# Performance work log

Measured on AMD Instinct MI355X. Metric: run time of the kernel, lower is better.

Reference implementation:

```python
import jax, jax.numpy as jnp
import numpy as np

N = 50000      # nodes
E = 800000     # edges (before self-loops)
DIN = 146      # input feature dim
D = 128        # hidden/out dim
G = 64         # graphs in batch
L = 4          # number of GCNConv layers (len(hidden_dims[1:]) + 1)
NC = 10        # classes
EPS = 1e-5     # BatchNorm eps


def setup_inputs() -> dict:
    key = jax.random.key(0)
    ks = jax.random.split(key, 12)
    x = jax.random.normal(ks[0], (N, DIN), jnp.float32)
    edge_index = jax.random.randint(ks[1], (2, E), 0, N, dtype=jnp.int64)
    batch = jnp.sort(jax.random.randint(ks[2], (N,), 0, G, dtype=jnp.int64))

    def lin(k, shape, fan_in):
        return (jax.random.normal(k, shape, jnp.float32) / np.sqrt(fan_in)).astype(jnp.float32)

    W_emb = lin(ks[3], (DIN, D), DIN)
    b_emb = jnp.zeros((D,), jnp.float32)
    W_gcn = lin(ks[4], (L, D, D), D)
    b_gcn = jnp.zeros((L, D), jnp.float32)
    bn_gamma = jnp.ones((L, D), jnp.float32)
    bn_beta = jnp.zeros((L, D), jnp.float32)
    W_r1 = lin(ks[5], (D, D // 2), D)
    b_r1 = jnp.zeros((D // 2,), jnp.float32)
    W_r2 = lin(ks[6], (D // 2, D // 4), D // 2)
    b_r2 = jnp.zeros((D // 4,), jnp.float32)
    W_r3 = lin(ks[7], (D // 4, NC), D // 4)
    b_r3 = jnp.zeros((NC,), jnp.float32)
    return {"x": x, "edge_index": edge_index, "batch": batch,
            "W_emb": W_emb, "b_emb": b_emb, "W_gcn": W_gcn, "b_gcn": b_gcn,
            "bn_gamma": bn_gamma, "bn_beta": bn_beta,
            "W_r1": W_r1, "b_r1": b_r1, "W_r2": W_r2, "b_r2": b_r2,
            "W_r3": W_r3, "b_r3": b_r3}


def reference(x, edge_index, batch, W_emb, b_emb, W_gcn, b_gcn,
              bn_gamma, bn_beta, W_r1, b_r1, W_r2, b_r2, W_r3, b_r3):
    # gcn_norm with self-loops (fill_value=1, improved=False)
    loop = jnp.arange(N, dtype=edge_index.dtype)
    src = jnp.concatenate([edge_index[0], loop])
    dst = jnp.concatenate([edge_index[1], loop])
    deg = jax.ops.segment_sum(jnp.ones(src.shape, x.dtype), dst, num_segments=N)
    dinv = jax.lax.rsqrt(jnp.maximum(deg, jnp.asarray(1e-12, x.dtype)))  # deg >= 1 (self loops)
    norm = (dinv[src] * dinv[dst])[:, None]  # [E+N, 1]

    h = x @ W_emb + b_emb  # embedding_h
    for l in range(L):
        h_in = h
        m = h @ W_gcn[l]                                            # [N, D]
        h = jax.ops.segment_sum(m[src] * norm, dst, num_segments=N) + b_gcn[l]
        # BatchNorm1d (training-mode batch stats, biased var)
        mu = h.mean(axis=0)
        var = h.var(axis=0)
        h = (h - mu) * jax.lax.rsqrt(var + EPS) * bn_gamma[l] + bn_beta[l]
        h = jax.nn.relu(h)
        h = h_in + h  # residual (dims always match here)

    # global_mean_pool over batch ids
    sums = jax.ops.segment_sum(h, batch, num_segments=G)
    cnts = jax.ops.segment_sum(jnp.ones((N, 1), h.dtype), batch, num_segments=G)
    hg = sums / jnp.maximum(cnts, 1.0)

    # MLPReadout: two hidden layers halving dims, then classifier
    z = jax.nn.relu(hg @ W_r1 + b_r1)
    z = jax.nn.relu(z @ W_r2 + b_r2)
    return z @ W_r3 + b_r3  # [G, NC]
```

## Files before the change

### kernel.cpp

```cpp
#include <hip/hip_runtime.h>
#include <hip/hip_bf16.h>

#define NN 50000
#define EE 800000
#define DIN 146
#define DD 128
#define GG 64
#define LL 4
#define NC 10
#define BN_EPS 1e-5f

#define KP_EMB 160
#define AST_L  136
#define NCOPY 64
#define NPW 2

#define NBKT 196
#define BHP  200
#define NBE  782

#define A_EDGE   NBE
#define A_INIT   (A_EDGE + 256)
#define A_REPACK (A_INIT + 3907)
#define A_BATCH  (A_REPACK + 196)
#define A_PARAMS (A_BATCH + 384)
#define A_WT     (A_PARAMS + 400)

#define B_GEMM 391
#define C_TOT  (B_GEMM + NBE)

typedef __attribute__((ext_vector_type(8))) short bf16x8;
typedef __attribute__((ext_vector_type(4))) float f32x4;

__device__ __forceinline__ float bf2f(__hip_bfloat16 v) { return __bfloat162float(v); }
__device__ __forceinline__ float loadf(const void* p, long i, int f32) {
    return f32 ? ((const float*)p)[i] : bf2f(((const __hip_bfloat16*)p)[i]);
}
__device__ __forceinline__ unsigned short f2bf_bits(float f) {
    __hip_bfloat16 h = __float2bfloat16(f);
    return *(unsigned short*)&h;
}
__device__ __forceinline__ float bfu2f(unsigned short u) {
    return __uint_as_float((unsigned)u << 16);
}
__device__ __forceinline__ float lo16(unsigned v) { return __uint_as_float(v << 16); }
__device__ __forceinline__ float hi16(unsigned v) { return __uint_as_float(v & 0xffff0000u); }
__device__ __forceinline__ float sload_f(const float* __restrict__ p, int j) {
    return __uint_as_float(__builtin_amdgcn_readfirstlane(__float_as_uint(p[j])));
}
__device__ __forceinline__ ushort4 pack4(f32x4 v) {
    ushort4 u;
    u.x = f2bf_bits(v[0]); u.y = f2bf_bits(v[1]);
    u.z = f2bf_bits(v[2]); u.w = f2bf_bits(v[3]);
    return u;
}

__device__ __forceinline__ int blk_excl_scan(int v, int t, int* wsum, int* total_sh) {
    __syncthreads();
    int lane = t & 63, w = t >> 6;
    int x = v;
    #pragma unroll
    for (int s = 1; s < 64; s <<= 1) {
        int y = __shfl_up(x, s, 64);
        if (lane >= s) x += y;
    }
    if (lane == 63) wsum[w] = x;
    __syncthreads();
    if (t == 0) {
// ... 244 lines not shown
    for (int t8 = 0; t8 < 8; ++t8) {
        #pragma unroll
        for (int c = 0; c < 5; ++c) {
            bf16x8 b = *(const bf16x8*)(Wt + (long)(t8 * 16 + m) * KP_EMB + c * 32 + quad * 8);
            acc[0][t8] = __builtin_amdgcn_mfma_f32_16x16x32_bf16(b, a[0][c], acc[0][t8], 0, 0, 0);
            acc[1][t8] = __builtin_amdgcn_mfma_f32_16x16x32_bf16(b, a[1][c], acc[1][t8], 0, 0, 0);
        }
    }
    #pragma unroll
    for (int rt = 0; rt < 2; ++rt) {
        int row = rbase + rt * 16 + m;
        int rloc = rl + rt * 16 + m;
        #pragma unroll
        for (int t8 = 0; t8 < 8; ++t8) {
            ushort4 u = pack4(acc[rt][t8]);
            *(ushort4*)(&sh.As[rloc * AST_L + t8 * 16 + quad * 4]) = u;
            if (row < n)
                *(ushort4*)(hb + (long)row * DD + t8 * 16 + quad * 4) = u;
        }
    }
    __syncthreads();
    bf16x8 a2[2][4];
    #pragma unroll
    for (int rt = 0; rt < 2; ++rt)
        #pragma unroll
        for (int c = 0; c < 4; ++c)
            a2[rt][c] = *(const bf16x8*)(&sh.As[(rl + rt * 16 + m) * AST_L + c * 32 + quad * 8]);
    f32x4 acc2[2][8];
    #pragma unroll
    for (int t8 = 0; t8 < 8; ++t8) {
        f32x4 z = {0.f, 0.f, 0.f, 0.f};
        acc2[0][t8] = z; acc2[1][t8] = z;
    }
    #pragma unroll
    for (int t8 = 0; t8 < 8; ++t8) {
        #pragma unroll
        for (int c = 0; c < 4; ++c) {
            bf16x8 b = *(const bf16x8*)(Wt0 + (long)(t8 * 16 + m) * DD + c * 32 + quad * 8);
            acc2[0][t8] = __builtin_amdgcn_mfma_f32_16x16x32_bf16(b, a2[0][c], acc2[0][t8], 0, 0, 0);
            acc2[1][t8] = __builtin_amdgcn_mfma_f32_16x16x32_bf16(b, a2[1][c], acc2[1][t8], 0, 0, 0);
        }
    }
    #pragma unroll
    for (int rt = 0; rt < 2; ++rt) {
        int row = rbase + rt * 16 + m;
        if (row < n) {
            #pragma unroll
            for (int t8 = 0; t8 < 8; ++t8)
                *(ushort4*)(Mb + (long)row * DD + t8 * 16 + quad * 4) = pack4(acc2[rt][t8]);
        }
    }
}

__global__ __launch_bounds__(256) void csr_kernel(
    const unsigned* __restrict__ bucketA, const int* __restrict__ base,
    int* __restrict__ off, float* __restrict__ dinv, int* __restrict__ src_s)
{
    __shared__ int dg[256], cur[256], wsum[4], total_sh;
    int b = blockIdx.x, t = threadIdx.x;
    int eb0 = base[b], eb1 = base[b + 1];
    dg[t] = 0;
    __syncthreads();
    for (int e = eb0 + t; e < eb1; e += 256)
        atomicAdd(&dg[bucketA[e] & 255u], 1);
    __syncthreads();
    int v = dg[t];
    int excl = blk_excl_scan(v, t, wsum, &total_sh);
    int node = b * 256 + t;
    if (node < NN) {
        off[node] = eb0 + excl;
        dinv[node] = rsqrtf((float)(v + 1));
    }
    cur[t] = excl;
    __syncthreads();
    for (int e = eb0 + t; e < eb1; e += 256) {
        unsigned pv = bucketA[e];
        int r = atomicAdd(&cur[pv & 255u], 1);
        src_s[eb0 + r] = (int)(pv >> 8);
    }
}

__global__ __launch_bounds__(256) void gemm_fused_kernel(
    const unsigned short* __restrict__ aggb, unsigned short* __restrict__ hb,
    const float* __restrict__ statmulti, const float* __restrict__ gamma,
    const float* __restrict__ beta,
    const unsigned short* __restrict__ Wt, unsigned short* __restrict__ Mb, int n)
{
    __shared__ unsigned short As[128 * AST_L];
    __shared__ float bnsh[256];
    int t = threadIdx.x;
    int r0 = blockIdx.x * 128;
    {
        float s = 0.0f;
        #pragma unroll 8
        for (int k = 0; k < NCOPY; ++k) s += statmulti[k * 256 + t];
        bnsh[t] = s;
    }
    __syncthreads();
    {
        int c4 = (t & 31) * 4, rsub = t >> 5;
        float inv_n = 1.0f / (float)n;
        float4 sm = *(const float4*)&bnsh[c4];
        float4 sq = *(const float4*)&bnsh[128 + c4];
        float4 ga = *(const float4*)&gamma[c4];
        float4 be = *(const float4*)&beta[c4];
        float4 mu, rs;
        mu.x = sm.x * inv_n; mu.y = sm.y * inv_n; mu.z = sm.z * inv_n; mu.w = sm.w * inv_n;
        rs.x = rsqrtf(sq.x * inv_n - mu.x * mu.x + BN_EPS) * ga.x;
        rs.y = rsqrtf(sq.y * inv_n - mu.y * mu.y + BN_EPS) * ga.y;
        rs.z = rsqrtf(sq.z * inv_n - mu.z * mu.z + BN_EPS) * ga.z;
        rs.w = rsqrtf(sq.w * inv_n - mu.w * mu.w + BN_EPS) * ga.w;
        #pragma unroll 4
        for (int i = 0; i < 16; ++i) {
            int row = i * 8 + rsub;
            int r = r0 + row;
            unsigned short o0 = 0, o1 = 0, o2 = 0, o3 = 0;
            if (r < n) {
                long g = (long)r * DD + c4;
                ushort4 au = *(const ushort4*)&aggb[g];
                ushort4 hu = *(const ushort4*)&hb[g];
                float h0 = bfu2f(hu.x) + fmaxf((bfu2f(au.x) - mu.x) * rs.x + be.x, 0.0f);
                float h1 = bfu2f(hu.y) + fmaxf((bfu2f(au.y) - mu.y) * rs.y + be.y, 0.0f);
                float h2 = bfu2f(hu.z) + fmaxf((bfu2f(au.z) - mu.z) * rs.z + be.z, 0.0f);
                float h3 = bfu2f(hu.w) + fmaxf((bfu2f(au.w) - mu.w) * rs.w + be.w, 0.0f);
                o0 = f2bf_bits(h0); o1 = f2bf_bits(h1);
                o2 = f2bf_bits(h2); o3 = f2bf_bits(h3);
                ushort4 ho; ho.x = o0; ho.y = o1; ho.z = o2; ho.w = o3;
                *(ushort4*)&hb[g] = ho;
            }
            unsigned short* dst = &As[row * AST_L + c4];
            dst[0] = o0; dst[1] = o1; dst[2] = o2; dst[3] = o3;
        }
    }
    __syncthreads();
    int lane = t & 63, w = t >> 6;
    int m = lane & 15, quad = lane >> 4;
    int rl = w * 32;
    int rbase = r0 + rl;
    bf16x8 a[2][4];
    #pragma unroll
    for (int rt = 0; rt < 2; ++rt)
        #pragma unroll
        for (int c = 0; c < 4; ++c)
            a[rt][c] = *(const bf16x8*)(As + (rl + rt * 16 + m) * AST_L + c * 32 + quad * 8);
    f32x4 acc[2][8];
    #pragma unroll
    for (int t8 = 0; t8 < 8; ++t8) {
        f32x4 z = {0.f, 0.f, 0.f, 0.f};
        acc[0][t8] = z; acc[1][t8] = z;
    }
    #pragma unroll
    for (int t8 = 0; t8 < 8; ++t8) {
        #pragma unroll
        for (int c = 0; c < 4; ++c) {
            bf16x8 b = *(const bf16x8*)(Wt + (long)(t8 * 16 + m) * DD + c * 32 + quad * 8);
            acc[0][t8] = __builtin_amdgcn_mfma_f32_16x16x32_bf16(b, a[0][c], acc[0][t8], 0, 0, 0);
            acc[1][t8] = __builtin_amdgcn_mfma_f32_16x16x32_bf16(b, a[1][c], acc[1][t8], 0, 0, 0);
        }
    }
    #pragma unroll
    for (int rt = 0; rt < 2; ++rt) {
        int row = rbase + rt * 16 + m;
        if (row < n) {
            #pragma unroll
            for (int t8 = 0; t8 < 8; ++t8)
                *(ushort4*)(Mb + (long)row * DD + t8 * 16 + quad * 4) = pack4(acc[rt][t8]);
        }
    }
}

__global__ __launch_bounds__(256) void agg_kernel(
    const unsigned* __restrict__ mb32, const int* __restrict__ off,
    const int* __restrict__ src_s,
    const float* __restrict__ dinv, const float* __restrict__ bias,
    unsigned* __restrict__ aggb32, float* __restrict__ statacc)
{
    __shared__ float2 ssum[4][64], ssq[4][64];
    int t = threadIdx.x;
    int wv = t >> 6, lane = t & 63;
    float2 bi = ((const float2*)bias)[lane];
    float2 sAcc = {0.0f, 0.0f}, qAcc = {0.0f, 0.0f};
    int i0 = (blockIdx.x * 4 + wv) * NPW;
    #pragma unroll 1
    for (int ni = 0; ni < NPW; ++ni) {
        int i = i0 + ni;
        if (i >= NN) break;
        int e  = __builtin_amdgcn_readfirstlane(off[i]);
        int e1 = __builtin_amdgcn_readfirstlane(off[i + 1]);
        float di = sload_f(dinv, i);
        unsigned vs = mb32[(long)i * 64 + lane];
        float a0 = di * lo16(vs), a1 = di * hi16(vs);
        for (; e + 8 <= e1; e += 8) {
            int j0 = __builtin_amdgcn_readfirstlane(src_s[e + 0]);
            int j1 = __builtin_amdgcn_readfirstlane(src_s[e + 1]);
            int j2 = __builtin_amdgcn_readfirstlane(src_s[e + 2]);
            int j3 = __builtin_amdgcn_readfirstlane(src_s[e + 3]);
            int j4 = __builtin_amdgcn_readfirstlane(src_s[e + 4]);
            int j5 = __builtin_amdgcn_readfirstlane(src_s[e + 5]);
            int j6 = __builtin_amdgcn_readfirstlane(src_s[e + 6]);
            int j7 = __builtin_amdgcn_readfirstlane(src_s[e + 7]);
            float d0 = sload_f(dinv, j0), d1 = sload_f(dinv, j1);
            float d2 = sload_f(dinv, j2), d3 = sload_f(dinv, j3);
            float d4 = sload_f(dinv, j4), d5 = sload_f(dinv, j5);
            float d6 = sload_f(dinv, j6), d7 = sload_f(dinv, j7);
            unsigned v0 = mb32[(long)j0 * 64 + lane];
            unsigned v1 = mb32[(long)j1 * 64 + lane];
            unsigned v2 = mb32[(long)j2 * 64 + lane];
            unsigned v3 = mb32[(long)j3 * 64 + lane];
            unsigned v4 = mb32[(long)j4 * 64 + lane];
            unsigned v5 = mb32[(long)j5 * 64 + lane];
            unsigned v6 = mb32[(long)j6 * 64 + lane];
            unsigned v7 = mb32[(long)j7 * 64 + lane];
            a0 = fmaf(d0, lo16(v0), a0); a1 = fmaf(d0, hi16(v0), a1);
            a0 = fmaf(d1, lo16(v1), a0); a1 = fmaf(d1, hi16(v1), a1);
            a0 = fmaf(d2, lo16(v2), a0); a1 = fmaf(d2, hi16(v2), a1);
            a0 = fmaf(d3, lo16(v3), a0); a1 = fmaf(d3, hi16(v3), a1);
            a0 = fmaf(d4, lo16(v4), a0); a1 = fmaf(d4, hi16(v4), a1);
            a0 = fmaf(d5, lo16(v5), a0); a1 = fmaf(d5, hi16(v5), a1);
            a0 = fmaf(d6, lo16(v6), a0); a1 = fmaf(d6, hi16(v6), a1);
            a0 = fmaf(d7, lo16(v7), a0); a1 = fmaf(d7, hi16(v7), a1);
        }
        for (; e + 4 <= e1; e += 4) {
            int j0 = __builtin_amdgcn_readfirstlane(src_s[e + 0]);
            int j1 = __builtin_amdgcn_readfirstlane(src_s[e + 1]);
            int j2 = __builtin_amdgcn_readfirstlane(src_s[e + 2]);
            int j3 = __builtin_amdgcn_readfirstlane(src_s[e + 3]);
            float d0 = sload_f(dinv, j0), d1 = sload_f(dinv, j1);
            float d2 = sload_f(dinv, j2), d3 = sload_f(dinv, j3);
            unsigned v0 = mb32[(long)j0 * 64 + lane];
            unsigned v1 = mb32[(long)j1 * 64 + lane];
            unsigned v2 = mb32[(long)j2 * 64 + lane];
            unsigned v3 = mb32[(long)j3 * 64 + lane];
            a0 = fmaf(d0, lo16(v0), a0); a1 = fmaf(d0, hi16(v0), a1);
            a0 = fmaf(d1, lo16(v1), a0); a1 = fmaf(d1, hi16(v1), a1);
            a0 = fmaf(d2, lo16(v2), a0); a1 = fmaf(d2, hi16(v2), a1);
            a0 = fmaf(d3, lo16(v3), a0); a1 = fmaf(d3, hi16(v3), a1);
        }
        for (; e < e1; ++e) {
            int j = __builtin_amdgcn_readfirstlane(src_s[e]);
            float dj = sload_f(dinv, j);
            unsigned v = mb32[(long)j * 64 + lane];
            a0 = fmaf(dj, lo16(v), a0); a1 = fmaf(dj, hi16(v), a1);
        }
        float o0 = fmaf(di, a0, bi.x);
        float o1 = fmaf(di, a1, bi.y);
        aggb32[(long)i * 64 + lane] = ((unsigned)f2bf_bits(o1) << 16) | f2bf_bits(o0);
        sAcc.x += o0; sAcc.y += o1;
        qAcc.x += o0 * o0; qAcc.y += o1 * o1;
    }
    ssum[wv][lane] = sAcc; ssq[wv][lane] = qAcc;
    __syncthreads();
    if (wv == 0) {
        float2 s0 = ssum[0][lane], s1 = ssum[1][lane], s2 = ssum[2][lane], s3 = ssum[3][lane];
        float2 q0 = ssq[0][lane], q1 = ssq[1][lane], q2 = ssq[2][lane], q3 = ssq[3][lane];
        float sx = s0.x + s1.x + s2.x + s3.x;
        float sy = s0.y + s1.y + s2.y + s3.y;
        float qx = q0.x + q1.x + q2.x + q3.x;
        float qy = q0.y + q1.y + q2.y + q3.y;
        float* copy = statacc + (blockIdx.x & (NCOPY - 1)) * 256;
        atomicAdd(&copy[2 * lane], sx);
        atomicAdd(&copy[2 * lane + 1], sy);
        atomicAdd(&copy[128 + 2 * lane], qx);
        atomicAdd(&copy[128 + 2 * lane + 1], qy);
    }
}

__global__ void pool1_kernel(const unsigned short* __restrict__ hb,
                             const unsigned short* __restrict__ aggb,
                             const float* __restrict__ statmulti,
                             const float* __restrict__ gamma, const float* __restrict__ beta,
                             const int* __restrict__ b32, float* __restrict__ hgsum, int n) {
    __shared__ float bnsh[256];
    int t = threadIdx.x;
    {
        float s = 0.0f;
        #pragma unroll 8
        for (int k = 0; k < NCOPY; ++k) s += statmulti[k * 256 + t];
        bnsh[t] = s;
    }
    __syncthreads();
    int c4 = (t & 31) * 4, rsub = t >> 5;
    float inv_n = 1.0f / (float)n;
    float4 sm = *(const float4*)&bnsh[c4];
    float4 sq = *(const float4*)&bnsh[128 + c4];
    float4 ga = *(const float4*)&gamma[c4];
    float4 be = *(const float4*)&beta[c4];
    float4 mu, rs;
    mu.x = sm.x * inv_n; mu.y = sm.y * inv_n; mu.z = sm.z * inv_n; mu.w = sm.w * inv_n;
    rs.x = rsqrtf(sq.x * inv_n - mu.x * mu.x + BN_EPS) * ga.x;
    rs.y = rsqrtf(sq.y * inv_n - mu.y * mu.y + BN_EPS) * ga.y;
    rs.z = rsqrtf(sq.z * inv_n - mu.z * mu.z + BN_EPS) * ga.z;
    rs.w = rsqrtf(sq.w * inv_n - mu.w * mu.w + BN_EPS) * ga.w;
    int rows_pb = (n + gridDim.x - 1) / gridDim.x;
    int r0 = blockIdx.x * rows_pb;
    int r1 = min(n, r0 + rows_pb);
    float4 acc = {0, 0, 0, 0};
    int gcur = -1;
    for (int r = r0 + rsub; r < r1; r += 8) {
        int g = b32[r];
        if (g != gcur) {
            if (gcur >= 0) {
                atomicAdd(&hgsum[gcur * DD + c4 + 0], acc.x);
                atomicAdd(&hgsum[gcur * DD + c4 + 1], acc.y);
                atomicAdd(&hgsum[gcur * DD + c4 + 2], acc.z);
                atomicAdd(&hgsum[gcur * DD + c4 + 3], acc.w);
            }
            acc.x = acc.y = acc.z = acc.w = 0.0f;
            gcur = ((unsigned)g < (unsigned)GG) ? g : -1;
        }
        if (gcur >= 0) {
            long ix = (long)r * DD + c4;
            ushort4 au = *(const ushort4*)&aggb[ix];
            ushort4 hu = *(const ushort4*)&hb[ix];
            acc.x += bfu2f(hu.x) + fmaxf((bfu2f(au.x) - mu.x) * rs.x + be.x, 0.0f);
            acc.y += bfu2f(hu.y) + fmaxf((bfu2f(au.y) - mu.y) * rs.y + be.y, 0.0f);
            acc.z += bfu2f(hu.z) + fmaxf((bfu2f(au.z) - mu.z) * rs.z + be.z, 0.0f);
            acc.w += bfu2f(hu.w) + fmaxf((bfu2f(au.w) - mu.w) * rs.w + be.w, 0.0f);
        }
    }
    if (gcur >= 0) {
        atomicAdd(&hgsum[gcur * DD + c4 + 0], acc.x);
        atomicAdd(&hgsum[gcur * DD + c4 + 1], acc.y);
        atomicAdd(&hgsum[gcur * DD + c4 + 2], acc.z);
        atomicAdd(&hgsum[gcur * DD + c4 + 3], acc.w);
    }
}

__device__ int lower_bound_i(const int* __restrict__ a, int n, int v) {
    int lo = 0, hi = n;
    while (lo < hi) {
        int mid = (lo + hi) >> 1;
        if (a[mid] < v) lo = mid + 1; else hi = mid;
    }
    return lo;
}

__global__ void readout_kernel(const float* __restrict__ hgsum, const int* __restrict__ b32,
                               const float* __restrict__ W1, const float* __restrict__ b1,
                               const float* __restrict__ W2, const float* __restrict__ b2,
                               const float* __restrict__ W3, const float* __restrict__ b3,
                               const int* __restrict__ flags, void* __restrict__ out, int n) {
    int f32 = flags[2];
    int g = blockIdx.x;
    int t = threadIdx.x;
    __shared__ float hgs[DD];
    __shared__ float z1[DD / 2];
    __shared__ float z2[DD / 4];
    int lo = lower_bound_i(b32, n, g);
    int hi = lower_bound_i(b32, n, g + 1);
    float invc = 1.0f / fmaxf((float)(hi - lo), 1.0f);
    hgs[t] = hgsum[g * DD + t] * invc;
    __syncthreads();
    if (t < DD / 2) {
        float acc = b1[t];
        #pragma unroll 8
        for (int k = 0; k < DD; ++k) acc = fmaf(hgs[k], W1[k * (DD / 2) + t], acc);
        z1[t] = fmaxf(acc, 0.0f);
    }
    __syncthreads();
    if (t < DD / 4) {
        float acc = b2[t];
        #pragma unroll 8
        for (int k = 0; k < DD / 2; ++k) acc = fmaf(z1[k], W2[k * (DD / 4) + t], acc);
        z2[t] = fmaxf(acc, 0.0f);
    }
    __syncthreads();
    if (t < NC) {
        float acc = b3[t];
        #pragma unroll 8
        for (int k = 0; k < DD / 4; ++k) acc = fmaf(z2[k], W3[k * NC + t], acc);
        if (f32) ((float*)out)[g * NC + t] = acc;
        else     ((__hip_bfloat16*)out)[g * NC + t] = __float2bfloat16(acc);
    }
}

extern "C" void kernel_launch(void* const* d_in, const int* in_sizes, int n_in,
                              void* d_out, int out_size, void* d_ws, size_t ws_size,
                              hipStream_t stream) {
    const void* x      = d_in[0];
    const void* ei     = d_in[1];
    const void* batch  = d_in[2];
    const void* W_emb  = d_in[3];
    const void* b_emb  = d_in[4];
    const void* W_gcn  = d_in[5];
    const void* b_gcn  = d_in[6];
    const void* bn_g   = d_in[7];
    const void* bn_b   = d_in[8];
    const void* W_r1   = d_in[9];
    const void* b_r1   = d_in[10];
    const void* W_r2   = d_in[11];
    const void* b_r2   = d_in[12];
    const void* W_r3   = d_in[13];
    const void* b_r3   = d_in[14];

    char* p = (char*)d_ws;
    auto alloc = [&](size_t bytes) -> void* {
        void* r = (void*)p;
        p += (bytes + 255) & ~(size_t)255;
        return r;
    };
    int*   flags  = (int*)alloc(64 * 4);
    int*   dcnt   = (int*)alloc(64 * 4);
    float* statmulti = (float*)alloc((size_t)LL * NCOPY * 256 * 4);
    float* hgsum  = (float*)alloc((size_t)GG * DD * 4);
    int*   off    = (int*)alloc((size_t)(NN + 1) * 4);
    float* dinv   = (float*)alloc((size_t)NN * 4);
    int*   b32    = (int*)alloc((size_t)NN * 4);
    int*   src_s  = (int*)alloc((size_t)EE * 4);
    unsigned* pk  = (unsigned*)alloc((size_t)EE * 4);
    unsigned char* bkt = (unsigned char*)alloc((size_t)EE);
    int*   bh     = (int*)alloc((size_t)NBE * BHP * 4);
    int*   tot    = (int*)alloc(256 * 4);
    int*   base   = (int*)alloc(256 * 4);
    unsigned* bucketA = (unsigned*)alloc((size_t)EE * 4);
    unsigned short* hb = (unsigned short*)alloc((size_t)NN * DD * 2);
    unsigned short* mb = (unsigned short*)alloc((size_t)NN * DD * 2);
    unsigned short* aggb = (unsigned short*)alloc((size_t)NN * DD * 2);
    unsigned short* xb = (unsigned short*)alloc((size_t)NN * KP_EMB * 2);
    unsigned short* wt_emb = (unsigned short*)alloc((size_t)DD * KP_EMB * 2);
    unsigned short* wt_gcn = (unsigned short*)alloc((size_t)LL * DD * DD * 2);
    float* b_emb32 = (float*)alloc(DD * 4);
    float* b_gcn32 = (float*)alloc((size_t)LL * DD * 4);
    float* bng32   = (float*)alloc((size_t)LL * DD * 4);
    float* bnb32   = (float*)alloc((size_t)LL * DD * 4);
    float* wr1     = (float*)alloc((size_t)DD * (DD / 2) * 4);
    float* br1     = (float*)alloc((DD / 2) * 4);
    float* wr2     = (float*)alloc((size_t)(DD / 2) * (DD / 4) * 4);
    float* br2     = (float*)alloc((DD / 4) * 4);
    float* wr3     = (float*)alloc((size_t)(DD / 4) * NC * 4);
    float* br3     = (float*)alloc(NC * 4);

    detect_kernel<<<1, 64, 0, stream>>>(ei, batch, W_emb, flags);

    Params12 P;
    P.p[0]  = { b_emb, b_emb32, DD, DD };
    P.p[1]  = { b_gcn, b_gcn32, LL * DD, LL * DD };
    P.p[2]  = { bn_g,  bng32,   LL * DD, LL * DD };
    P.p[3]  = { bn_b,  bnb32,   LL * DD, LL * DD };
    P.p[4]  = { W_r1,  wr1,     DD * (DD / 2), DD * (DD / 2) };
    P.p[5]  = { b_r1,  br1,     DD / 2, DD / 2 };
    P.p[6]  = { W_r2,  wr2,     (DD / 2) * (DD / 4), (DD / 2) * (DD / 4) };
    P.p[7]  = { b_r2,  br2,     DD / 4, DD / 4 };
    P.p[8]  = { W_r3,  wr3,     (DD / 4) * NC, (DD / 4) * NC };
    P.p[9]  = { b_r3,  br3,     NC, NC };
    P.p[10] = { b_r3,  br3,     0, 0 };
    P.p[11] = { b_r3,  br3,     0, 0 };

    WtDescs5 W;
    W.p[0] = { W_emb, 0,            wt_emb,                DIN, KP_EMB };
    W.p[1] = { W_gcn, 0L * DD * DD, wt_gcn + 0L * DD * DD, DD,  DD };
    W.p[2] = { W_gcn, 1L * DD * DD, wt_gcn + 1L * DD * DD, DD,  DD };
    W.p[3] = { W_gcn, 2L * DD * DD, wt_gcn + 2L * DD * DD, DD,  DD };
    W.p[4] = { W_gcn, 3L * DD * DD, wt_gcn + 3L * DD * DD, DD,  DD };

    mega_conv_kernel<<<A_WT, 256, 0, stream>>>(x, ei, batch, flags, xb, statmulti,
                                               hgsum, b32, pk, bkt, bh, dcnt, P, W);

    bscan_kernel<<<NBKT, 256, 0, stream>>>(bh, tot, base, off + NN, dcnt);

    bucket_emb_kernel<<<C_TOT, 256, 0, stream>>>(pk, bkt, bh, base, bucketA,
                                                 xb, wt_emb, wt_gcn, b_emb32, hb, mb, NN);

    csr_kernel<<<NBKT, 256, 0, stream>>>(bucketA, base, off, dinv, src_s);

    int ngemm = (NN + 127) / 128;
    int nagg = (NN + 4 * NPW - 1) / (4 * NPW);
    for (int l = 0; l < LL; ++l) {
        if (l > 0) {
            gemm_fused_kernel<<<ngemm, 256, 0, stream>>>(
                aggb, hb, statmulti + (size_t)(l - 1) * NCOPY * 256,
                bng32 + (l - 1) * DD, bnb32 + (l - 1) * DD,
                wt_gcn + (size_t)l * DD * DD, mb, NN);
        }
        agg_kernel<<<nagg, 256, 0, stream>>>((const unsigned*)mb, off, src_s, dinv,
                                             b_gcn32 + l * DD, (unsigned*)aggb,
                                             statmulti + (size_t)l * NCOPY * 256);
    }

    pool1_kernel<<<512, 256, 0, stream>>>(hb, aggb, statmulti + (size_t)(LL - 1) * NCOPY * 256,
                                          bng32 + (LL - 1) * DD, bnb32 + (LL - 1) * DD,
                                          b32, hgsum, NN);
    readout_kernel<<<GG, DD, 0, stream>>>(hgsum, b32, wr1, br1, wr2, br2, wr3, br3,
                                          flags, d_out, NN);
}
```

Measured before the change: 405.8 us.

## Fuse CSR build, GCN layers, pooling and readout into one cooperative persistent kernel

```diff
diff --git a/kernel.cpp b/kernel.cpp
--- a/kernel.cpp
+++ b/kernel.cpp
@@ -1,5 +1,8 @@
 #include <hip/hip_runtime.h>
 #include <hip/hip_bf16.h>
+#include <hip/hip_cooperative_groups.h>
+
+namespace cg = cooperative_groups;
 
 #define NN 50000
 #define EE 800000
@@ -13,7 +16,7 @@
 #define KP_EMB 160
 #define AST_L  136
 #define NCOPY 64
-#define NPW 2
+#define NT_GEMM 391
 
 #define NBKT 196
 #define BHP  200
@@ -364,56 +367,263 @@
     }
 }
 
-__global__ __launch_bounds__(256) void csr_kernel(
-    const unsigned* __restrict__ bucketA, const int* __restrict__ base,
-    int* __restrict__ off, float* __restrict__ dinv, int* __restrict__ src_s)
-{
-    __shared__ int dg[256], cur[256], wsum[4], total_sh;
-    int b = blockIdx.x, t = threadIdx.x;
-    int eb0 = base[b], eb1 = base[b + 1];
-    dg[t] = 0;
-    __syncthreads();
-    for (int e = eb0 + t; e < eb1; e += 256)
-        atomicAdd(&dg[bucketA[e] & 255u], 1);
-    __syncthreads();
-    int v = dg[t];
-    int excl = blk_excl_scan(v, t, wsum, &total_sh);
-    int node = b * 256 + t;
-    if (node < NN) {
-        off[node] = eb0 + excl;
-        dinv[node] = rsqrtf((float)(v + 1));
-    }
-    cur[t] = excl;
-    __syncthreads();
-    for (int e = eb0 + t; e < eb1; e += 256) {
-        unsigned pv = bucketA[e];
-        int r = atomicAdd(&cur[pv & 255u], 1);
-        src_s[eb0 + r] = (int)(pv >> 8);
-    }
-}
-
-__global__ __launch_bounds__(256) void gemm_fused_kernel(
-    const unsigned short* __restrict__ aggb, unsigned short* __restrict__ hb,
-    const float* __restrict__ statmulti, const float* __restrict__ gamma,
-    const float* __restrict__ beta,
-    const unsigned short* __restrict__ Wt, unsigned short* __restrict__ Mb, int n)
-{
-    __shared__ unsigned short As[128 * AST_L];
-    __shared__ float bnsh[256];
+__device__ __forceinline__ int lower_bound_i(const int* __restrict__ a, int n, int v) {
+    int lo = 0, hi = n;
+    while (lo < hi) {
+        int mid = (lo + hi) >> 1;
+        if (a[mid] < v) lo = mid + 1; else hi = mid;
+    }
+    return lo;
+}
+
+struct LayersArgs {
+    const unsigned* bucketA; const int* base;
+    int* off; float* dinv; int* src_s;
+    unsigned short* aggb; unsigned short* hb;
+    float* statmulti;
+    const float* bng; const float* bnb;
+    const unsigned short* wt_gcn;
+    unsigned short* mb;
+    const float* bgcn;
+    const int* b32; float* hgsum;
+    const float* W1; const float* b1; const float* W2; const float* b2;
+    const float* W3; const float* b3;
+    const int* flags; void* out; int n;
+};
+
+__global__ __launch_bounds__(256, 3) void layers_kernel(LayersArgs A) {
+    cg::grid_group grid = cg::this_grid();
+    __shared__ union {
+        struct { unsigned short As[128 * AST_L]; float bnsh[256]; } g;
+        struct { float2 ssum[4][64]; float2 ssq[4][64]; } a;
+        struct { int dg[256]; int cur[256]; int wsum[4]; int total; } c;
+        struct { float hgs[DD]; float z1[DD / 2]; float z2[DD / 4]; } r;
+    } sh;
     int t = threadIdx.x;
-    int r0 = blockIdx.x * 128;
+    int n = A.n;
+    int lane = t & 63, wv = t >> 6;
+    int m = lane & 15, quad = lane >> 4;
+    int rl = wv * 32;
+
+    for (int b = blockIdx.x; b < NBKT; b += gridDim.x) {
+        int eb0 = A.base[b], eb1 = A.base[b + 1];
+        sh.c.dg[t] = 0;
+        __syncthreads();
+        for (int e = eb0 + t; e < eb1; e += 256)
+            atomicAdd(&sh.c.dg[A.bucketA[e] & 255u], 1);
+        __syncthreads();
+        int v = sh.c.dg[t];
+        int excl = blk_excl_scan(v, t, sh.c.wsum, &sh.c.total);
+        int node = b * 256 + t;
+        if (node < NN) {
+            A.off[node] = eb0 + excl;
+            A.dinv[node] = rsqrtf((float)(v + 1));
+        }
+        sh.c.cur[t] = excl;
+        __syncthreads();
+        for (int e = eb0 + t; e < eb1; e += 256) {
+            unsigned pv = A.bucketA[e];
+            int r = atomicAdd(&sh.c.cur[pv & 255u], 1);
+            A.src_s[eb0 + r] = (int)(pv >> 8);
+        }
+        __syncthreads();
+    }
+    grid.sync();
+
+    const unsigned* mb32 = (const unsigned*)A.mb;
+    unsigned* aggb32 = (unsigned*)A.aggb;
+
+    for (int l = 0; l < LL; ++l) {
+        if (l > 0) {
+            const float* statm = A.statmulti + (size_t)(l - 1) * NCOPY * 256;
+            const float* gamma = A.bng + (size_t)(l - 1) * DD;
+            const float* beta  = A.bnb + (size_t)(l - 1) * DD;
+            const unsigned short* Wt = A.wt_gcn + (size_t)l * DD * DD;
+            {
+                float s = 0.0f;
+                #pragma unroll 8
+                for (int k = 0; k < NCOPY; ++k) s += statm[k * 256 + t];
+                sh.g.bnsh[t] = s;
+            }
+            __syncthreads();
+            int c4 = (t & 31) * 4, rsub = t >> 5;
+            float inv_n = 1.0f / (float)n;
+            float4 sm = *(const float4*)&sh.g.bnsh[c4];
+            float4 sq = *(const float4*)&sh.g.bnsh[128 + c4];
+            float4 ga = *(const float4*)&gamma[c4];
+            float4 be = *(const float4*)&beta[c4];
+            float4 mu, rs;
+            mu.x = sm.x * inv_n; mu.y = sm.y * inv_n; mu.z = sm.z * inv_n; mu.w = sm.w * inv_n;
+            rs.x = rsqrtf(sq.x * inv_n - mu.x * mu.x + BN_EPS) * ga.x;
+            rs.y = rsqrtf(sq.y * inv_n - mu.y * mu.y + BN_EPS) * ga.y;
+            rs.z = rsqrtf(sq.z * inv_n - mu.z * mu.z + BN_EPS) * ga.z;
+            rs.w = rsqrtf(sq.w * inv_n - mu.w * mu.w + BN_EPS) * ga.w;
+            for (int tile = blockIdx.x; tile < NT_GEMM; tile += gridDim.x) {
+                int r0 = tile * 128;
+                __syncthreads();
+                #pragma unroll 4
+                for (int i = 0; i < 16; ++i) {
+                    int row = i * 8 + rsub;
+                    int r = r0 + row;
+                    unsigned short o0 = 0, o1 = 0, o2 = 0, o3 = 0;
+                    if (r < n) {
+                        long g = (long)r * DD + c4;
+                        ushort4 au = *(const ushort4*)&A.aggb[g];
+                        ushort4 hu = *(const ushort4*)&A.hb[g];
+                        float h0 = bfu2f(hu.x) + fmaxf((bfu2f(au.x) - mu.x) * rs.x + be.x, 0.0f);
+                        float h1 = bfu2f(hu.y) + fmaxf((bfu2f(au.y) - mu.y) * rs.y + be.y, 0.0f);
+                        float h2 = bfu2f(hu.z) + fmaxf((bfu2f(au.z) - mu.z) * rs.z + be.z, 0.0f);
+                        float h3 = bfu2f(hu.w) + fmaxf((bfu2f(au.w) - mu.w) * rs.w + be.w, 0.0f);
+                        o0 = f2bf_bits(h0); o1 = f2bf_bits(h1);
+                        o2 = f2bf_bits(h2); o3 = f2bf_bits(h3);
+                        ushort4 ho; ho.x = o0; ho.y = o1; ho.z = o2; ho.w = o3;
+                        *(ushort4*)&A.hb[g] = ho;
+                    }
+                    unsigned short* dst = &sh.g.As[row * AST_L + c4];
+                    dst[0] = o0; dst[1] = o1; dst[2] = o2; dst[3] = o3;
+                }
+                __syncthreads();
+                int rbase = r0 + rl;
+                bf16x8 a[2][4];
+                #pragma unroll
+                for (int rt = 0; rt < 2; ++rt)
+                    #pragma unroll
+                    for (int c = 0; c < 4; ++c)
+                        a[rt][c] = *(const bf16x8*)(&sh.g.As[(rl + rt * 16 + m) * AST_L + c * 32 + quad * 8]);
+                f32x4 acc[2][8];
+                #pragma unroll
+                for (int t8 = 0; t8 < 8; ++t8) {
+                    f32x4 z = {0.f, 0.f, 0.f, 0.f};
+                    acc[0][t8] = z; acc[1][t8] = z;
+                }
+                #pragma unroll
+                for (int t8 = 0; t8 < 8; ++t8) {
+                    #pragma unroll
+                    for (int c = 0; c < 4; ++c) {
+                        bf16x8 b = *(const bf16x8*)(Wt + (long)(t8 * 16 + m) * DD + c * 32 + quad * 8);
+                        acc[0][t8] = __builtin_amdgcn_mfma_f32_16x16x32_bf16(b, a[0][c], acc[0][t8], 0, 0, 0);
+                        acc[1][t8] = __builtin_amdgcn_mfma_f32_16x16x32_bf16(b, a[1][c], acc[1][t8], 0, 0, 0);
+                    }
+                }
+                #pragma unroll
+                for (int rt = 0; rt < 2; ++rt) {
+                    int row = rbase + rt * 16 + m;
+                    if (row < n) {
+                        #pragma unroll
+                        for (int t8 = 0; t8 < 8; ++t8)
+                            *(ushort4*)(A.mb + (long)row * DD + t8 * 16 + quad * 4) = pack4(acc[rt][t8]);
+                    }
+                }
+            }
+            grid.sync();
+        }
+        {
+            const float* bias = A.bgcn + (size_t)l * DD;
+            float* statacc = A.statmulti + (size_t)l * NCOPY * 256;
+            float2 bi = ((const float2*)bias)[lane];
+            float2 sAcc = {0.0f, 0.0f}, qAcc = {0.0f, 0.0f};
+            int wstep = gridDim.x * 4;
+            for (int i = blockIdx.x * 4 + wv; i < n; i += wstep) {
+                int e  = __builtin_amdgcn_readfirstlane(A.off[i]);
+                int e1 = __builtin_amdgcn_readfirstlane(A.off[i + 1]);
+                float di = sload_f(A.dinv, i);
+                unsigned vs = mb32[(long)i * 64 + lane];
+                float a0 = di * lo16(vs), a1 = di * hi16(vs);
+                for (; e + 8 <= e1; e += 8) {
+                    int j0 = __builtin_amdgcn_readfirstlane(A.src_s[e + 0]);
+                    int j1 = __builtin_amdgcn_readfirstlane(A.src_s[e + 1]);
+                    int j2 = __builtin_amdgcn_readfirstlane(A.src_s[e + 2]);
+                    int j3 = __builtin_amdgcn_readfirstlane(A.src_s[e + 3]);
+                    int j4 = __builtin_amdgcn_readfirstlane(A.src_s[e + 4]);
+                    int j5 = __builtin_amdgcn_readfirstlane(A.src_s[e + 5]);
+                    int j6 = __builtin_amdgcn_readfirstlane(A.src_s[e + 6]);
+                    int j7 = __builtin_amdgcn_readfirstlane(A.src_s[e + 7]);
+                    float d0 = sload_f(A.dinv, j0), d1 = sload_f(A.dinv, j1);
+                    float d2 = sload_f(A.dinv, j2), d3 = sload_f(A.dinv, j3);
+                    float d4 = sload_f(A.dinv, j4), d5 = sload_f(A.dinv, j5);
+                    float d6 = sload_f(A.dinv, j6), d7 = sload_f(A.dinv, j7);
+                    unsigned v0 = mb32[(long)j0 * 64 + lane];
+                    unsigned v1 = mb32[(long)j1 * 64 + lane];
+                    unsigned v2 = mb32[(long)j2 * 64 + lane];
+                    unsigned v3 = mb32[(long)j3 * 64 + lane];
+                    unsigned v4 = mb32[(long)j4 * 64 + lane];
+                    unsigned v5 = mb32[(long)j5 * 64 + lane];
+                    unsigned v6 = mb32[(long)j6 * 64 + lane];
+                    unsigned v7 = mb32[(long)j7 * 64 + lane];
+                    a0 = fmaf(d0, lo16(v0), a0); a1 = fmaf(d0, hi16(v0), a1);
+                    a0 = fmaf(d1, lo16(v1), a0); a1 = fmaf(d1, hi16(v1), a1);
+                    a0 = fmaf(d2, lo16(v2), a0); a1 = fmaf(d2, hi16(v2), a1);
+                    a0 = fmaf(d3, lo16(v3), a0); a1 = fmaf(d3, hi16(v3), a1);
+                    a0 = fmaf(d4, lo16(v4), a0); a1 = fmaf(d4, hi16(v4), a1);
+                    a0 = fmaf(d5, lo16(v5), a0); a1 = fmaf(d5, hi16(v5), a1);
+                    a0 = fmaf(d6, lo16(v6), a0); a1 = fmaf(d6, hi16(v6), a1);
+                    a0 = fmaf(d7, lo16(v7), a0); a1 = fmaf(d7, hi16(v7), a1);
+                }
+                for (; e + 4 <= e1; e += 4) {
+                    int j0 = __builtin_amdgcn_readfirstlane(A.src_s[e + 0]);
+                    int j1 = __builtin_amdgcn_readfirstlane(A.src_s[e + 1]);
+                    int j2 = __builtin_amdgcn_readfirstlane(A.src_s[e + 2]);
+                    int j3 = __builtin_amdgcn_readfirstlane(A.src_s[e + 3]);
+                    float d0 = sload_f(A.dinv, j0), d1 = sload_f(A.dinv, j1);
+                    float d2 = sload_f(A.dinv, j2), d3 = sload_f(A.dinv, j3);
+                    unsigned v0 = mb32[(long)j0 * 64 + lane];
+                    unsigned v1 = mb32[(long)j1 * 64 + lane];
+                    unsigned v2 = mb32[(long)j2 * 64 + lane];
+                    unsigned v3 = mb32[(long)j3 * 64 + lane];
+                    a0 = fmaf(d0, lo16(v0), a0); a1 = fmaf(d0, hi16(v0), a1);
+                    a0 = fmaf(d1, lo16(v1), a0); a1 = fmaf(d1, hi16(v1), a1);
+                    a0 = fmaf(d2, lo16(v2), a0); a1 = fmaf(d2, hi16(v2), a1);
+                    a0 = fmaf(d3, lo16(v3), a0); a1 = fmaf(d3, hi16(v3), a1);
+                }
+                for (; e < e1; ++e) {
+                    int j = __builtin_amdgcn_readfirstlane(A.src_s[e]);
+                    float dj = sload_f(A.dinv, j);
+                    unsigned v = mb32[(long)j * 64 + lane];
+                    a0 = fmaf(dj, lo16(v), a0); a1 = fmaf(dj, hi16(v), a1);
+                }
+                float o0 = fmaf(di, a0, bi.x);
+                float o1 = fmaf(di, a1, bi.y);
+                aggb32[(long)i * 64 + lane] = ((unsigned)f2bf_bits(o1) << 16) | f2bf_bits(o0);
+                sAcc.x += o0; sAcc.y += o1;
+                qAcc.x += o0 * o0; qAcc.y += o1 * o1;
+            }
+            __syncthreads();
+            sh.a.ssum[wv][lane] = sAcc; sh.a.ssq[wv][lane] = qAcc;
+            __syncthreads();
+            if (wv == 0) {
+                float2 s0 = sh.a.ssum[0][lane], s1 = sh.a.ssum[1][lane];
+                float2 s2 = sh.a.ssum[2][lane], s3 = sh.a.ssum[3][lane];
+                float2 q0 = sh.a.ssq[0][lane], q1 = sh.a.ssq[1][lane];
+                float2 q2 = sh.a.ssq[2][lane], q3 = sh.a.ssq[3][lane];
+                float sx = s0.x + s1.x + s2.x + s3.x;
+                float sy = s0.y + s1.y + s2.y + s3.y;
+                float qx = q0.x + q1.x + q2.x + q3.x;
+                float qy = q0.y + q1.y + q2.y + q3.y;
+                float* copy = statacc + (blockIdx.x & (NCOPY - 1)) * 256;
+                atomicAdd(&copy[2 * lane], sx);
+                atomicAdd(&copy[2 * lane + 1], sy);
+                atomicAdd(&copy[128 + 2 * lane], qx);
+                atomicAdd(&copy[128 + 2 * lane + 1], qy);
+            }
+        }
+        grid.sync();
+    }
+
     {
-        float s = 0.0f;
-        #pragma unroll 8
-        for (int k = 0; k < NCOPY; ++k) s += statmulti[k * 256 + t];
-        bnsh[t] = s;
-    }
-    __syncthreads();
-    {
+        const float* statm = A.statmulti + (size_t)(LL - 1) * NCOPY * 256;
+        const float* gamma = A.bng + (size_t)(LL - 1) * DD;
+        const float* beta  = A.bnb + (size_t)(LL - 1) * DD;
+        {
+            float s = 0.0f;
+            #pragma unroll 8
+            for (int k = 0; k < NCOPY; ++k) s += statm[k * 256 + t];
+            sh.g.bnsh[t] = s;
+        }
+        __syncthreads();
         int c4 = (t & 31) * 4, rsub = t >> 5;
         float inv_n = 1.0f / (float)n;
-        float4 sm = *(const float4*)&bnsh[c4];
-        float4 sq = *(const float4*)&bnsh[128 + c4];
+        float4 sm = *(const float4*)&sh.g.bnsh[c4];
+        float4 sq = *(const float4*)&sh.g.bnsh[128 + c4];
         float4 ga = *(const float4*)&gamma[c4];
         float4 be = *(const float4*)&beta[c4];
         float4 mu, rs;
@@ -422,267 +632,73 @@
         rs.y = rsqrtf(sq.y * inv_n - mu.y * mu.y + BN_EPS) * ga.y;
         rs.z = rsqrtf(sq.z * inv_n - mu.z * mu.z + BN_EPS) * ga.z;
         rs.w = rsqrtf(sq.w * inv_n - mu.w * mu.w + BN_EPS) * ga.w;
-        #pragma unroll 4
-        for (int i = 0; i < 16; ++i) {
-            int row = i * 8 + rsub;
-            int r = r0 + row;
-            unsigned short o0 = 0, o1 = 0, o2 = 0, o3 = 0;
-            if (r < n) {
-                long g = (long)r * DD + c4;
-                ushort4 au = *(const ushort4*)&aggb[g];
-                ushort4 hu = *(const ushort4*)&hb[g];
-                float h0 = bfu2f(hu.x) + fmaxf((bfu2f(au.x) - mu.x) * rs.x + be.x, 0.0f);
-                float h1 = bfu2f(hu.y) + fmaxf((bfu2f(au.y) - mu.y) * rs.y + be.y, 0.0f);
-                float h2 = bfu2f(hu.z) + fmaxf((bfu2f(au.z) - mu.z) * rs.z + be.z, 0.0f);
-                float h3 = bfu2f(hu.w) + fmaxf((bfu2f(au.w) - mu.w) * rs.w + be.w, 0.0f);
-                o0 = f2bf_bits(h0); o1 = f2bf_bits(h1);
-                o2 = f2bf_bits(h2); o3 = f2bf_bits(h3);
-                ushort4 ho; ho.x = o0; ho.y = o1; ho.z = o2; ho.w = o3;
-                *(ushort4*)&hb[g] = ho;
-            }
-            unsigned short* dst = &As[row * AST_L + c4];
-            dst[0] = o0; dst[1] = o1; dst[2] = o2; dst[3] = o3;
-        }
-    }
-    __syncthreads();
-    int lane = t & 63, w = t >> 6;
-    int m = lane & 15, quad = lane >> 4;
-    int rl = w * 32;
-    int rbase = r0 + rl;
-    bf16x8 a[2][4];
-    #pragma unroll
-    for (int rt = 0; rt < 2; ++rt)
-        #pragma unroll
-        for (int c = 0; c < 4; ++c)
-            a[rt][c] = *(const bf16x8*)(As + (rl + rt * 16 + m) * AST_L + c * 32 + quad * 8);
-    f32x4 acc[2][8];
-    #pragma unroll
-    for (int t8 = 0; t8 < 8; ++t8) {
-        f32x4 z = {0.f, 0.f, 0.f, 0.f};
-        acc[0][t8] = z; acc[1][t8] = z;
-    }
-    #pragma unroll
-    for (int t8 = 0; t8 < 8; ++t8) {
-        #pragma unroll
-        for (int c = 0; c < 4; ++c) {
-            bf16x8 b = *(const bf16x8*)(Wt + (long)(t8 * 16 + m) * DD + c * 32 + quad * 8);
-            acc[0][t8] = __builtin_amdgcn_mfma_f32_16x16x32_bf16(b, a[0][c], acc[0][t8], 0, 0, 0);
-            acc[1][t8] = __builtin_amdgcn_mfma_f32_16x16x32_bf16(b, a[1][c], acc[1][t8], 0, 0, 0);
-        }
-    }
-    #pragma unroll
-    for (int rt = 0; rt < 2; ++rt) {
-        int row = rbase + rt * 16 + m;
-        if (row < n) {
-            #pragma unroll
-            for (int t8 = 0; t8 < 8; ++t8)
-                *(ushort4*)(Mb + (long)row * DD + t8 * 16 + quad * 4) = pack4(acc[rt][t8]);
-        }
-    }
-}
-
-__global__ __launch_bounds__(256) void agg_kernel(
-    const unsigned* __restrict__ mb32, const int* __restrict__ off,
-    const int* __restrict__ src_s,
-    const float* __restrict__ dinv, const float* __restrict__ bias,
-    unsigned* __restrict__ aggb32, float* __restrict__ statacc)
-{
-    __shared__ float2 ssum[4][64], ssq[4][64];
-    int t = threadIdx.x;
-    int wv = t >> 6, lane = t & 63;
-    float2 bi = ((const float2*)bias)[lane];
-    float2 sAcc = {0.0f, 0.0f}, qAcc = {0.0f, 0.0f};
-    int i0 = (blockIdx.x * 4 + wv) * NPW;
-    #pragma unroll 1
-    for (int ni = 0; ni < NPW; ++ni) {
-        int i = i0 + ni;
-        if (i >= NN) break;
-        int e  = __builtin_amdgcn_readfirstlane(off[i]);
-        int e1 = __builtin_amdgcn_readfirstlane(off[i + 1]);
-        float di = sload_f(dinv, i);
-        unsigned vs = mb32[(long)i * 64 + lane];
-        float a0 = di * lo16(vs), a1 = di * hi16(vs);
-        for (; e + 8 <= e1; e += 8) {
-            int j0 = __builtin_amdgcn_readfirstlane(src_s[e + 0]);
-            int j1 = __builtin_amdgcn_readfirstlane(src_s[e + 1]);
-            int j2 = __builtin_amdgcn_readfirstlane(src_s[e + 2]);
-            int j3 = __builtin_amdgcn_readfirstlane(src_s[e + 3]);
-            int j4 = __builtin_amdgcn_readfirstlane(src_s[e + 4]);
-            int j5 = __builtin_amdgcn_readfirstlane(src_s[e + 5]);
-            int j6 = __builtin_amdgcn_readfirstlane(src_s[e + 6]);
-            int j7 = __builtin_amdgcn_readfirstlane(src_s[e + 7]);
-            float d0 = sload_f(dinv, j0), d1 = sload_f(dinv, j1);
-            float d2 = sload_f(dinv, j2), d3 = sload_f(dinv, j3);
-            float d4 = sload_f(dinv, j4), d5 = sload_f(dinv, j5);
-            float d6 = sload_f(dinv, j6), d7 = sload_f(dinv, j7);
-            unsigned v0 = mb32[(long)j0 * 64 + lane];
-            unsigned v1 = mb32[(long)j1 * 64 + lane];
-            unsigned v2 = mb32[(long)j2 * 64 + lane];
-            unsigned v3 = mb32[(long)j3 * 64 + lane];
-            unsigned v4 = mb32[(long)j4 * 64 + lane];
-            unsigned v5 = mb32[(long)j5 * 64 + lane];
-            unsigned v6 = mb32[(long)j6 * 64 + lane];
-            unsigned v7 = mb32[(long)j7 * 64 + lane];
-            a0 = fmaf(d0, lo16(v0), a0); a1 = fmaf(d0, hi16(v0), a1);
-            a0 = fmaf(d1, lo16(v1), a0); a1 = fmaf(d1, hi16(v1), a1);
-            a0 = fmaf(d2, lo16(v2), a0); a1 = fmaf(d2, hi16(v2), a1);
-            a0 = fmaf(d3, lo16(v3), a0); a1 = fmaf(d3, hi16(v3), a1);
-            a0 = fmaf(d4, lo16(v4), a0); a1 = fmaf(d4, hi16(v4), a1);
-            a0 = fmaf(d5, lo16(v5), a0); a1 = fmaf(d5, hi16(v5), a1);
-            a0 = fmaf(d6, lo16(v6), a0); a1 = fmaf(d6, hi16(v6), a1);
-            a0 = fmaf(d7, lo16(v7), a0); a1 = fmaf(d7, hi16(v7), a1);
-        }
-        for (; e + 4 <= e1; e += 4) {
-            int j0 = __builtin_amdgcn_readfirstlane(src_s[e + 0]);
-            int j1 = __builtin_amdgcn_readfirstlane(src_s[e + 1]);
-            int j2 = __builtin_amdgcn_readfirstlane(src_s[e + 2]);
-            int j3 = __builtin_amdgcn_readfirstlane(src_s[e + 3]);
-            float d0 = sload_f(dinv, j0), d1 = sload_f(dinv, j1);
-            float d2 = sload_f(dinv, j2), d3 = sload_f(dinv, j3);
-            unsigned v0 = mb32[(long)j0 * 64 + lane];
-            unsigned v1 = mb32[(long)j1 * 64 + lane];
-            unsigned v2 = mb32[(long)j2 * 64 + lane];
-            unsigned v3 = mb32[(long)j3 * 64 + lane];
-            a0 = fmaf(d0, lo16(v0), a0); a1 = fmaf(d0, hi16(v0), a1);
-            a0 = fmaf(d1, lo16(v1), a0); a1 = fmaf(d1, hi16(v1), a1);
-            a0 = fmaf(d2, lo16(v2), a0); a1 = fmaf(d2, hi16(v2), a1);
-            a0 = fmaf(d3, lo16(v3), a0); a1 = fmaf(d3, hi16(v3), a1);
-        }
-        for (; e < e1; ++e) {
-            int j = __builtin_amdgcn_readfirstlane(src_s[e]);
-            float dj = sload_f(dinv, j);
-            unsigned v = mb32[(long)j * 64 + lane];
-            a0 = fmaf(dj, lo16(v), a0); a1 = fmaf(dj, hi16(v), a1);
-        }
-        float o0 = fmaf(di, a0, bi.x);
-        float o1 = fmaf(di, a1, bi.y);
-        aggb32[(long)i * 64 + lane] = ((unsigned)f2bf_bits(o1) << 16) | f2bf_bits(o0);
-        sAcc.x += o0; sAcc.y += o1;
-        qAcc.x += o0 * o0; qAcc.y += o1 * o1;
-    }
-    ssum[wv][lane] = sAcc; ssq[wv][lane] = qAcc;
-    __syncthreads();
-    if (wv == 0) {
-        float2 s0 = ssum[0][lane], s1 = ssum[1][lane], s2 = ssum[2][lane], s3 = ssum[3][lane];
-        float2 q0 = ssq[0][lane], q1 = ssq[1][lane], q2 = ssq[2][lane], q3 = ssq[3][lane];
-        float sx = s0.x + s1.x + s2.x + s3.x;
-        float sy = s0.y + s1.y + s2.y + s3.y;
-        float qx = q0.x + q1.x + q2.x + q3.x;
-        float qy = q0.y + q1.y + q2.y + q3.y;
-        float* copy = statacc + (blockIdx.x & (NCOPY - 1)) * 256;
-        atomicAdd(&copy[2 * lane], sx);
-        atomicAdd(&copy[2 * lane + 1], sy);
-        atomicAdd(&copy[128 + 2 * lane], qx);
-        atomicAdd(&copy[128 + 2 * lane + 1], qy);
-    }
-}
-
-__global__ void pool1_kernel(const unsigned short* __restrict__ hb,
-                             const unsigned short* __restrict__ aggb,
-                             const float* __restrict__ statmulti,
-                             const float* __restrict__ gamma, const float* __restrict__ beta,
-                             const int* __restrict__ b32, float* __restrict__ hgsum, int n) {
-    __shared__ float bnsh[256];
-    int t = threadIdx.x;
-    {
-        float s = 0.0f;
-        #pragma unroll 8
-        for (int k = 0; k < NCOPY; ++k) s += statmulti[k * 256 + t];
-        bnsh[t] = s;
-    }
-    __syncthreads();
-    int c4 = (t & 31) * 4, rsub = t >> 5;
-    float inv_n = 1.0f / (float)n;
-    float4 sm = *(const float4*)&bnsh[c4];
-    float4 sq = *(const float4*)&bnsh[128 + c4];
-    float4 ga = *(const float4*)&gamma[c4];
-    float4 be = *(const float4*)&beta[c4];
-    float4 mu, rs;
-    mu.x = sm.x * inv_n; mu.y = sm.y * inv_n; mu.z = sm.z * inv_n; mu.w = sm.w * inv_n;
-    rs.x = rsqrtf(sq.x * inv_n - mu.x * mu.x + BN_EPS) * ga.x;
-    rs.y = rsqrtf(sq.y * inv_n - mu.y * mu.y + BN_EPS) * ga.y;
-    rs.z = rsqrtf(sq.z * inv_n - mu.z * mu.z + BN_EPS) * ga.z;
-    rs.w = rsqrtf(sq.w * inv_n - mu.w * mu.w + BN_EPS) * ga.w;
-    int rows_pb = (n + gridDim.x - 1) / gridDim.x;
-    int r0 = blockIdx.x * rows_pb;
-    int r1 = min(n, r0 + rows_pb);
-    float4 acc = {0, 0, 0, 0};
-    int gcur = -1;
-    for (int r = r0 + rsub; r < r1; r += 8) {
-        int g = b32[r];
-        if (g != gcur) {
+        int rows_pb = (n + gridDim.x - 1) / gridDim.x;
+        int r0 = blockIdx.x * rows_pb;
+        int r1 = min(n, r0 + rows_pb);
+        float4 acc = {0, 0, 0, 0};
+        int gcur = -1;
+        for (int r = r0 + rsub; r < r1; r += 8) {
+            int g = A.b32[r];
+            if (g != gcur) {
+                if (gcur >= 0) {
+                    atomicAdd(&A.hgsum[gcur * DD + c4 + 0], acc.x);
+                    atomicAdd(&A.hgsum[gcur * DD + c4 + 1], acc.y);
+                    atomicAdd(&A.hgsum[gcur * DD + c4 + 2], acc.z);
+                    atomicAdd(&A.hgsum[gcur * DD + c4 + 3], acc.w);
+                }
+                acc.x = acc.y = acc.z = acc.w = 0.0f;
+                gcur = ((unsigned)g < (unsigned)GG) ? g : -1;
+            }
             if (gcur >= 0) {
-                atomicAdd(&hgsum[gcur * DD + c4 + 0], acc.x);
-                atomicAdd(&hgsum[gcur * DD + c4 + 1], acc.y);
-                atomicAdd(&hgsum[gcur * DD + c4 + 2], acc.z);
-                atomicAdd(&hgsum[gcur * DD + c4 + 3], acc.w);
-            }
-            acc.x = acc.y = acc.z = acc.w = 0.0f;
-            gcur = ((unsigned)g < (unsigned)GG) ? g : -1;
+                long ix = (long)r * DD + c4;
+                ushort4 au = *(const ushort4*)&A.aggb[ix];
+                ushort4 hu = *(const ushort4*)&A.hb[ix];
+                acc.x += bfu2f(hu.x) + fmaxf((bfu2f(au.x) - mu.x) * rs.x + be.x, 0.0f);
+                acc.y += bfu2f(hu.y) + fmaxf((bfu2f(au.y) - mu.y) * rs.y + be.y, 0.0f);
+                acc.z += bfu2f(hu.z) + fmaxf((bfu2f(au.z) - mu.z) * rs.z + be.z, 0.0f);
+                acc.w += bfu2f(hu.w) + fmaxf((bfu2f(au.w) - mu.w) * rs.w + be.w, 0.0f);
+            }
         }
         if (gcur >= 0) {
-            long ix = (long)r * DD + c4;
-            ushort4 au = *(const ushort4*)&aggb[ix];
-            ushort4 hu = *(const ushort4*)&hb[ix];
-            acc.x += bfu2f(hu.x) + fmaxf((bfu2f(au.x) - mu.x) * rs.x + be.x, 0.0f);
-            acc.y += bfu2f(hu.y) + fmaxf((bfu2f(au.y) - mu.y) * rs.y + be.y, 0.0f);
-            acc.z += bfu2f(hu.z) + fmaxf((bfu2f(au.z) - mu.z) * rs.z + be.z, 0.0f);
-            acc.w += bfu2f(hu.w) + fmaxf((bfu2f(au.w) - mu.w) * rs.w + be.w, 0.0f);
-        }
-    }
-    if (gcur >= 0) {
-        atomicAdd(&hgsum[gcur * DD + c4 + 0], acc.x);
-        atomicAdd(&hgsum[gcur * DD + c4 + 1], acc.y);
-        atomicAdd(&hgsum[gcur * DD + c4 + 2], acc.z);
-        atomicAdd(&hgsum[gcur * DD + c4 + 3], acc.w);
-    }
-}
-
-__device__ int lower_bound_i(const int* __restrict__ a, int n, int v) {
-    int lo = 0, hi = n;
-    while (lo < hi) {
-        int mid = (lo + hi) >> 1;
-        if (a[mid] < v) lo = mid + 1; else hi = mid;
-    }
-    return lo;
-}
-
-__global__ void readout_kernel(const float* __restrict__ hgsum, const int* __restrict__ b32,
-                               const float* __restrict__ W1, const float* __restrict__ b1,
-                               const float* __restrict__ W2, const float* __restrict__ b2,
-                               const float* __restrict__ W3, const float* __restrict__ b3,
-                               const int* __restrict__ flags, void* __restrict__ out, int n) {
-    int f32 = flags[2];
-    int g = blockIdx.x;
-    int t = threadIdx.x;
-    __shared__ float hgs[DD];
-    __shared__ float z1[DD / 2];
-    __shared__ float z2[DD / 4];
-    int lo = lower_bound_i(b32, n, g);
-    int hi = lower_bound_i(b32, n, g + 1);
-    float invc = 1.0f / fmaxf((float)(hi - lo), 1.0f);
-    hgs[t] = hgsum[g * DD + t] * invc;
-    __syncthreads();
-    if (t < DD / 2) {
-        float acc = b1[t];
-        #pragma unroll 8
-        for (int k = 0; k < DD; ++k) acc = fmaf(hgs[k], W1[k * (DD / 2) + t], acc);
-        z1[t] = fmaxf(acc, 0.0f);
-    }
-    __syncthreads();
-    if (t < DD / 4) {
-        float acc = b2[t];
-        #pragma unroll 8
-        for (int k = 0; k < DD / 2; ++k) acc = fmaf(z1[k], W2[k * (DD / 4) + t], acc);
-        z2[t] = fmaxf(acc, 0.0f);
-    }
-    __syncthreads();
-    if (t < NC) {
-        float acc = b3[t];
-        #pragma unroll 8
-        for (int k = 0; k < DD / 4; ++k) acc = fmaf(z2[k], W3[k * NC + t], acc);
-        if (f32) ((float*)out)[g * NC + t] = acc;
-        else     ((__hip_bfloat16*)out)[g * NC + t] = __float2bfloat16(acc);
+            atomicAdd(&A.hgsum[gcur * DD + c4 + 0], acc.x);
+            atomicAdd(&A.hgsum[gcur * DD + c4 + 1], acc.y);
+            atomicAdd(&A.hgsum[gcur * DD + c4 + 2], acc.z);
+            atomicAdd(&A.hgsum[gcur * DD + c4 + 3], acc.w);
+        }
+    }
+    grid.sync();
+
+    if (blockIdx.x < GG) {
+        int g = blockIdx.x;
+        int f32 = A.flags[2];
+        if (t < DD) {
+            int lo = lower_bound_i(A.b32, n, g);
+            int hi = lower_bound_i(A.b32, n, g + 1);
+            float invc = 1.0f / fmaxf((float)(hi - lo), 1.0f);
+            sh.r.hgs[t] = A.hgsum[g * DD + t] * invc;
+        }
+        __syncthreads();
+        if (t < DD / 2) {
+            float acc = A.b1[t];
+            #pragma unroll 8
+            for (int k = 0; k < DD; ++k) acc = fmaf(sh.r.hgs[k], A.W1[k * (DD / 2) + t], acc);
+            sh.r.z1[t] = fmaxf(acc, 0.0f);
+        }
+        __syncthreads();
+        if (t < DD / 4) {
+            float acc = A.b2[t];
+            #pragma unroll 8
+            for (int k = 0; k < DD / 2; ++k) acc = fmaf(sh.r.z1[k], A.W2[k * (DD / 4) + t], acc);
+            sh.r.z2[t] = fmaxf(acc, 0.0f);
+        }
+        __syncthreads();
+        if (t < NC) {
+            float acc = A.b3[t];
+            #pragma unroll 8
+            for (int k = 0; k < DD / 4; ++k) acc = fmaf(sh.r.z2[k], A.W3[k * NC + t], acc);
+            if (f32) ((float*)A.out)[g * NC + t] = acc;
+            else     ((__hip_bfloat16*)A.out)[g * NC + t] = __float2bfloat16(acc);
+        }
     }
 }
 
@@ -773,25 +789,32 @@
     bucket_emb_kernel<<<C_TOT, 256, 0, stream>>>(pk, bkt, bh, base, bucketA,
                                                  xb, wt_emb, wt_gcn, b_emb32, hb, mb, NN);
 
-    csr_kernel<<<NBKT, 256, 0, stream>>>(bucketA, base, off, dinv, src_s);
-
-    int ngemm = (NN + 127) / 128;
-    int nagg = (NN + 4 * NPW - 1) / (4 * NPW);
-    for (int l = 0; l < LL; ++l) {
-        if (l > 0) {
-            gemm_fused_kernel<<<ngemm, 256, 0, stream>>>(
-                aggb, hb, statmulti + (size_t)(l - 1) * NCOPY * 256,
-                bng32 + (l - 1) * DD, bnb32 + (l - 1) * DD,
-                wt_gcn + (size_t)l * DD * DD, mb, NN);
-        }
-        agg_kernel<<<nagg, 256, 0, stream>>>((const unsigned*)mb, off, src_s, dinv,
-                                             b_gcn32 + l * DD, (unsigned*)aggb,
-                                             statmulti + (size_t)l * NCOPY * 256);
-    }
-
-    pool1_kernel<<<512, 256, 0, stream>>>(hb, aggb, statmulti + (size_t)(LL - 1) * NCOPY * 256,
-                                          bng32 + (LL - 1) * DD, bnb32 + (LL - 1) * DD,
-                                          b32, hgsum, NN);
-    readout_kernel<<<GG, DD, 0, stream>>>(hgsum, b32, wr1, br1, wr2, br2, wr3, br3,
-                                          flags, d_out, NN);
-}
+    static int s_grid = 0;
+    if (s_grid == 0) {
+        int mb_per_cu = 0;
+        hipOccupancyMaxActiveBlocksPerMultiprocessor(&mb_per_cu, layers_kernel, 256, 0);
+        if (mb_per_cu < 1) mb_per_cu = 1;
+        hipDeviceProp_t prop;
+        int ncu = 256;
+        if (hipGetDeviceProperties(&prop, 0) == hipSuccess && prop.multiProcessorCount > 0)
+            ncu = prop.multiProcessorCount;
+        s_grid = ncu * mb_per_cu;
+        if (s_grid < GG) s_grid = GG;
+    }
+    LayersArgs LA;
+    LA.bucketA = bucketA; LA.base = base;
+    LA.off = off; LA.dinv = dinv; LA.src_s = src_s;
+    LA.aggb = aggb; LA.hb = hb;
+    LA.statmulti = statmulti;
+    LA.bng = bng32; LA.bnb = bnb32;
+    LA.wt_gcn = wt_gcn;
+    LA.mb = mb;
+    LA.bgcn = b_gcn32;
+    LA.b32 = b32; LA.hgsum = hgsum;
+    LA.W1 = wr1; LA.b1 = br1; LA.W2 = wr2; LA.b2 = br2;
+    LA.W3 = wr3; LA.b3 = br3;
+    LA.flags = flags; LA.out = d_out; LA.n = NN;
+    void* kargs[] = { (void*)&LA };
+    hipLaunchCooperativeKernel((const void*)layers_kernel, dim3(s_grid), dim3(256),
+                               kargs, 0, stream);
+}
```

New measurement: 1.125 ms. +177.3%, slower.
